# Optimization experiments

Measured on AMD Instinct MI355X. Metric: run time of the kernel, lower is better.

Reference implementation:

```python
import jax, jax.numpy as jnp
import numpy as np

LMAX, MMAX = 4, 2
C_IN, C_OUT = 128, 128           # sphere_channels, m_output_channels
NUM_EXPERTS = 8
NUM_SYSTEMS = 16
NUM_EDGES = 12288
M_SIZE = [LMAX + 1, 2 * (LMAX - 1 + 1), 2 * (LMAX - 2 + 1)]  # [5, 8, 6]


def _mole_linear(x, W, ce, b=None):
    """MoLE linear: per-edge expert mixing of weights, equivalently mixing of
    per-expert outputs.  x: [N, in] or [N, 2, in]; W: [K, in, out]; ce: [N, K]."""
    if x.ndim == 2:
        z = jnp.einsum('ni,kio->nko', x, W)        # [N, K, out]
        y = jnp.einsum('nk,nko->no', ce, z)
    else:
        z = jnp.einsum('nci,kio->nkco', x, W)      # [N, K, 2, out]
        y = jnp.einsum('nk,nkco->nco', ce, z)
    if b is not None:
        y = y + ce @ b                              # mixed bias, b: [K, out]
    return y


def setup_inputs() -> dict:
    key = jax.random.key(0)
    ks = jax.random.split(key, 8)
    num_mcoef = sum(M_SIZE)  # 19
    x = jax.random.normal(ks[0], (NUM_EDGES, num_mcoef, C_IN), dtype=jnp.float32)
    x_edge = jax.random.normal(ks[1], (NUM_EDGES, C_IN), dtype=jnp.float32)
    expert_coefficients = jax.random.uniform(ks[2], (NUM_SYSTEMS, NUM_EXPERTS), dtype=jnp.float32)
    edge_batch = jax.random.randint(ks[3], (NUM_EDGES,), 0, NUM_SYSTEMS)
    # fc_m0: in = (lmax+1)*C, out = (lmax+1)*C_out, with bias
    in0 = (LMAX + 1) * C_IN
    out0 = (LMAX + 1) * C_OUT
    W_m0 = jax.random.normal(ks[4], (NUM_EXPERTS, in0, out0), dtype=jnp.float32) * 0.02
    b_m0 = jnp.zeros((NUM_EXPERTS, out0), dtype=jnp.float32)
    # so2_m_conv m: in = (lmax-m+1)*C, out = 2*(lmax-m+1)*C_out, no bias
    nc1 = LMAX - 1 + 1
    W_m1 = jax.random.normal(ks[5], (NUM_EXPERTS, nc1 * C_IN, 2 * nc1 * C_OUT), dtype=jnp.float32) * 0.02
    nc2 = LMAX - 2 + 1
    W_m2 = jax.random.normal(ks[6], (NUM_EXPERTS, nc2 * C_IN, 2 * nc2 * C_OUT), dtype=jnp.float32) * 0.02
    return {
        'x': x, 'x_edge': x_edge,
        'expert_coefficients': expert_coefficients, 'edge_batch': edge_batch,
        'W_m0': W_m0, 'b_m0': b_m0, 'W_m1': W_m1, 'W_m2': W_m2,
    }


def reference(x, x_edge, expert_coefficients, edge_batch, W_m0, b_m0, W_m1, W_m2):
    N = x.shape[0]
    ce = expert_coefficients[edge_batch]               # [N, K] per-edge mix coeffs
    x0, x1, x2 = jnp.split(x, np.cumsum(M_SIZE[:-1]), axis=1)
    # m = 0 branch (internal_weights=True -> no radial rescale)
    y0 = _mole_linear(x0.reshape(N, -1), W_m0, ce, b_m0)
    out = [y0.reshape(N, -1, C_OUT)]                   # [N, lmax+1, C_out]
    # m >= 1 branches: SO(2) real/imag recombination
    for m, Wm, xm in ((1, W_m1, x1), (2, W_m2, x2)):
        nc = LMAX - m + 1
        xm = xm.reshape(N, 2, nc * C_IN)
        ym = _mole_linear(xm, Wm, ce)                  # [N, 2, 2*nc*C_out]
        ym = ym.reshape(N, 4, nc * C_OUT)
        x_m_r = ym[:, 0] - ym[:, 3]                    # x_r_0 - x_i_1
        x_m_i = ym[:, 2] + ym[:, 1]                    # x_r_1 + x_i_0
        out.append(x_m_r.reshape(N, nc, C_OUT))
        out.append(x_m_i.reshape(N, nc, C_OUT))
    return jnp.concatenate(out, axis=1)                # [N, 19, C_out]
```

## Files before the change

kernel.cpp:

```cpp
#include <hip/hip_runtime.h>
#include <cstdint>

#define N_EDGES 12288
#define ROWLEN  2432
#define CAP     2048

typedef __bf16 bf16;
typedef __bf16 bf16x8 __attribute__((ext_vector_type(8)));
typedef __bf16 bf16x4 __attribute__((ext_vector_type(4)));
typedef float  f32x4  __attribute__((ext_vector_type(4)));

#define ELEMS0 (640*640)
#define ELEMS1 (1024*1024)
#define ELEMS2 (768*768)

#define WS_IDX_OFF   1024
#define WS_BIAS_OFF  (WS_IDX_OFF + 16*CAP*4)
#define WS_W_OFF     (WS_BIAS_OFF + 16*640*4)
#define WZ_ELEMS     ((size_t)16*(ELEMS0+ELEMS1+ELEMS2))

template<int B> struct Cfg;
template<> struct Cfg<0> { static constexpr int K=640,  KS=640, XOFF=0,    NT=5;
                           static constexpr size_t WOFF=0; };
template<> struct Cfg<1> { static constexpr int K=1024, KS=512, XOFF=640,  NT=8;
                           static constexpr size_t WOFF=(size_t)16*ELEMS0; };
template<> struct Cfg<2> { static constexpr int K=768,  KS=384, XOFF=1664, NT=6;
                           static constexpr size_t WOFF=(size_t)16*ELEMS0+(size_t)16*ELEMS1; };

__device__ __forceinline__ void async_copy16(const void* g, void* l) {
  auto gp = reinterpret_cast<const __attribute__((address_space(1))) unsigned int*>(
      reinterpret_cast<uintptr_t>(g));
  auto lp = reinterpret_cast<__attribute__((address_space(3))) unsigned int*>(
      (unsigned int)reinterpret_cast<uintptr_t>(l));
  __builtin_amdgcn_global_load_lds(gp, lp, 16, 0, 0);
}

template<int B>
__device__ __forceinline__ void mix_body(const float* __restrict__ Wsrc,
                                         const float* ce_s,
                                         unsigned short* __restrict__ Wz, int pos) {
  constexpr int N = Cfg<B>::K, KS = Cfg<B>::KS, NT = N / 128, HALF = N / 2;
  constexpr int SRC_STRIDE = KS * N;
  constexpr size_t DST_STRIDE = (size_t)Cfg<B>::K * N;
  int nn = pos & 127, kgrp = (pos >> 7) & 3, rest = pos >> 9;
  int nt = rest % NT, kblk = rest / NT;
  int i0 = kblk * 32 + kgrp * 8;
  int c  = nt * 128 + nn;
  int si = i0, sc = c; float sg = 1.f;
  if (B > 0 && i0 >= KS) {
    si = i0 - KS;
    if (c < HALF) { sc = c + HALF; sg = -1.f; } else { sc = c - HALF; }
  }
  float w[8][8];
  const float* p0 = Wsrc + (size_t)si * N + sc;
#pragma unroll
  for (int e = 0; e < 8; ++e) {
    const float* p = p0 + (size_t)e * SRC_STRIDE;
#pragma unroll
    for (int j = 0; j < 8; ++j)
      w[e][j] = sg * p[(size_t)j * N];
  }
  unsigned short* db = Wz + Cfg<B>::WOFF + (size_t)pos * 8;
#pragma unroll
  for (int s = 0; s < 16; ++s) {
    float a[8] = {0, 0, 0, 0, 0, 0, 0, 0};
#pragma unroll
    for (int e = 0; e < 8; ++e) {
      float cc = ce_s[s * 8 + e];
#pragma unroll
      for (int j = 0; j < 8; ++j) a[j] += cc * w[e][j];
    }
    bf16x8 v;
#pragma unroll
    for (int j = 0; j < 8; ++j) v[j] = (bf16)a[j];
    *(bf16x8*)(db + s * DST_STRIDE) = v;
  }
}

__global__ __launch_bounds__(256) void prep_all(
    const float* __restrict__ W0, const float* __restrict__ W1,
    const float* __restrict__ W2, const float* __restrict__ ce,
    unsigned short* __restrict__ Wz,
    const int* __restrict__ eb, int* __restrict__ counts, int* __restrict__ idxb,
    const float* __restrict__ b0, float* __restrict__ bias) {
  __shared__ float ce_s[128];
  __shared__ int hcnt[16], hbase[16];
  int tid = threadIdx.x;
  int bx = blockIdx.x;
  if (bx < 1000) {
    if (tid < 128) ce_s[tid] = ce[tid];
    __syncthreads();
    if (bx < 200)      mix_body<0>(W0, ce_s, Wz, bx * 256 + tid);
    else if (bx < 712) mix_body<1>(W1, ce_s, Wz, (bx - 200) * 256 + tid);
    else               mix_body<2>(W2, ce_s, Wz, (bx - 712) * 256 + tid);
  } else if (bx < 1048) {
    int t = (bx - 1000) * 256 + tid;
    if (tid < 16) hcnt[tid] = 0;
    __syncthreads();
    int s = -1, lp = 0;
    if (t < N_EDGES) { s = eb[t]; lp = atomicAdd(&hcnt[s], 1); }
    __syncthreads();
    if (tid < 16) hbase[tid] = atomicAdd(counts + tid, hcnt[tid]);
    __syncthreads();
    if (s >= 0) { int p = hbase[s] + lp; if (p < CAP) idxb[s * CAP + p] = t; }
  } else {
    int t = (bx - 1048) * 256 + tid;
    int s = t / 640, c = t - s * 640;
    float a = 0.f;
#pragma unroll
    for (int e = 0; e < 8; ++e) a += ce[s * 8 + e] * b0[e * 640 + c];
    bias[t] = a;
  }
}

template<int B>
__device__ __forceinline__ void gemm_body(
    const float* __restrict__ x, const char* __restrict__ zeros,
    const unsigned short* __restrict__ Wz,
    const int* __restrict__ counts, const int* __restrict__ idxb,
    const float* __restrict__ bias, float* __restrict__ out,
    int s, int mt, int nt2, char* sm, int* eidx)
{
  constexpr int K = Cfg<B>::K, NT = Cfg<B>::NT, KB = K / 32, XOFF = Cfg<B>::XOFF;
  static_assert((K / 32) % 2 == 0, "KB must be even for the 2x-unrolled loop");
  int cnt = counts[s];
  int m0 = mt * 128;
  if (m0 >= cnt) return;
  int tid = threadIdx.x;
  if (tid < 128) eidx[tid] = (m0 + tid < cnt) ? idxb[s * CAP + m0 + tid] : -1;
  __syncthreads();
  char* Acur = sm;          char* Anxt = sm + 8192;
  char* Bc = sm + 16384;    char* Bm = sm + 32768;    char* Bn = sm + 49152;
  int wv = tid >> 6, ln = tid & 63;
  int wm = wv >> 1, wn = wv & 1;
  int kq = ln >> 4, lm = ln & 15;
  int c0 = nt2 * 2;
  int c16 = tid & 7, rbase = tid >> 3;
  int kq_w = c16 >> 1, half = c16 & 1;
  const char* arow4[4]; int kinc4[4];
#pragma unroll
  for (int i = 0; i < 4; ++i) {
    int e = eidx[rbase + 32 * i];
    if (e >= 0) { arow4[i] = (const char*)(x + (size_t)e * ROWLEN + XOFF); kinc4[i] = 128; }
    else        { arow4[i] = zeros; kinc4[i] = 0; }
  }
  const unsigned short* wb = Wz + Cfg<B>::WOFF + (size_t)s * K * K;

  auto loadA2 = [&](int kb, f32x4& r0, f32x4& r1, f32x4& r2, f32x4& r3)
      __attribute__((always_inline)) {
    r0 = *(const f32x4*)(arow4[0] + (size_t)kb * kinc4[0] + c16 * 16);
    r1 = *(const f32x4*)(arow4[1] + (size_t)kb * kinc4[1] + c16 * 16);
    r2 = *(const f32x4*)(arow4[2] + (size_t)kb * kinc4[2] + c16 * 16);
    r3 = *(const f32x4*)(arow4[3] + (size_t)kb * kinc4[3] + c16 * 16);
  };
  auto writeA2 = [&](char* dst, f32x4& r0, f32x4& r1, f32x4& r2, f32x4& r3)
      __attribute__((always_inline)) {
    f32x4 rr[4] = {r0, r1, r2, r3};
#pragma unroll
    for (int i = 0; i < 4; ++i) {
      int r = rbase + 32 * i;
      bf16x4 v;
      v[0] = (bf16)rr[i][0]; v[1] = (bf16)rr[i][1];
      v[2] = (bf16)rr[i][2]; v[3] = (bf16)rr[i][3];
      *(bf16x4*)(dst + kq_w * 2048 + ((r ^ (kq_w << 1)) * 16) + half * 8) = v;
    }
  };
  auto stageB = [&](int kb, char* dst) __attribute__((always_inline)) {
    const unsigned short* base = wb + (size_t)kb * (NT * 4096);
#pragma unroll
    for (int i = 0; i < 4; ++i) {
      int c = i * 256 + tid;
      int ck = c0 + (c >> 9); if (ck > NT - 1) ck = NT - 1;
      async_copy16(base + (size_t)ck * 4096 + (c & 511) * 8,
                   dst + (i * 256 + wv * 64) * 16);
    }
  };

  f32x4 acc[4][8];
#pragma unroll
  for (int i = 0; i < 4; ++i)
#pragma unroll
    for (int j = 0; j < 8; ++j) {
      acc[i][j][0] = 0.f; acc[i][j][1] = 0.f; acc[i][j][2] = 0.f; acc[i][j][3] = 0.f;
    }

  auto kstep = [&](int kb, f32x4& o0, f32x4& o1, f32x4& o2, f32x4& o3,
                           f32x4& n0, f32x4& n1, f32x4& n2, f32x4& n3)
      __attribute__((always_inline)) {
    if (kb + 2 < KB) {
      stageB(kb + 2, Bn);
      loadA2(kb + 2, n0, n1, n2, n3);
    }
    __builtin_amdgcn_sched_barrier(0);
    bf16x8 af[4], bq[8];
#pragma unroll
    for (int mi = 0; mi < 4; ++mi) {
      int r = wm * 64 + mi * 16 + lm;
      af[mi] = *(const bf16x8*)(Acur + kq * 2048 + ((r ^ (kq << 1)) * 16));
    }
#pragma unroll
    for (int ni = 0; ni < 8; ++ni)
      bq[ni] = *(const bf16x8*)(Bc + wn * 8192 + kq * 2048 + (ni * 16 + lm) * 16);
    __builtin_amdgcn_s_setprio(1);
#pragma unroll
    for (int mi = 0; mi < 4; ++mi)
#pragma unroll
      for (int ni = 0; ni < 8; ++ni)
        acc[mi][ni] = __builtin_amdgcn_mfma_f32_16x16x32_bf16(af[mi], bq[ni], acc[mi][ni], 0, 0, 0);
    __builtin_amdgcn_s_setprio(0);
    if (kb + 1 < KB)
      writeA2(Anxt, o0, o1, o2, o3);
    asm volatile("s_waitcnt lgkmcnt(0)" ::: "memory");
    __builtin_amdgcn_s_barrier();
    __builtin_amdgcn_sched_barrier(0);
    { char* t = Acur; Acur = Anxt; Anxt = t; }
    { char* tb = Bc; Bc = Bm; Bm = Bn; Bn = tb; }
  };

  f32x4 a0, a1, a2, a3, b0, b1, b2, b3;
  stageB(0, Bc);
  loadA2(0, a0, a1, a2, a3);
  writeA2(Acur, a0, a1, a2, a3);
  stageB(1, Bm);
  loadA2(1, a0, a1, a2, a3);
  asm volatile("s_waitcnt lgkmcnt(0)" ::: "memory");
  __builtin_amdgcn_s_barrier();
  __builtin_amdgcn_sched_barrier(0);

#pragma unroll 1
  for (int kb = 0; kb < KB; kb += 2) {
    kstep(kb,     a0, a1, a2, a3,  b0, b1, b2, b3);
    kstep(kb + 1, b0, b1, b2, b3,  a0, a1, a2, a3);
  }
  int cc = c0 + wn;
  if (cc >= NT) return;
  float bv[8] = {0, 0, 0, 0, 0, 0, 0, 0};
  if (B == 0) {
#pragma unroll
    for (int ni = 0; ni < 8; ++ni)
      bv[ni] = bias[s * 640 + cc * 128 + ni * 16 + lm];
  }
#pragma unroll
  for (int mi = 0; mi < 4; ++mi) {
#pragma unroll
    for (int r = 0; r < 4; ++r) {
      int row = wm * 64 + mi * 16 + kq * 4 + r;
      int e = eidx[row];
      if (e < 0) continue;
      float* po = out + (size_t)e * ROWLEN + XOFF + cc * 128 + lm;
#pragma unroll
      for (int ni = 0; ni < 8; ++ni) po[ni * 16] = acc[mi][ni][r] + bv[ni];
    }
  }
}

__global__ __launch_bounds__(256, 2) void gemm_all(
    const float* __restrict__ x, const char* __restrict__ zeros,
    const unsigned short* __restrict__ Wz,
    const int* __restrict__ counts, const int* __restrict__ idxb,
    const float* __restrict__ bias, float* __restrict__ out) {
  extern __shared__ char sm[];
  __shared__ int eidx[128];
  int g = blockIdx.x;
  int xcd = g & 7, j = g >> 3;
  int s = xcd + 8 * (j / 160);
  int r = j % 160;
  int mt = r / 10, bx = r % 10;
  if (bx < 3)      gemm_body<0>(x, zeros, Wz, counts, idxb, bias, out, s, mt, bx,     sm, eidx);
  else if (bx < 7) gemm_body<1>(x, zeros, Wz, counts, idxb, bias, out, s, mt, bx - 3, sm, eidx);
  else             gemm_body<2>(x, zeros, Wz, counts, idxb, bias, out, s, mt, bx - 7, sm, eidx);
}

extern "C" void kernel_launch(void* const* d_in, const int* in_sizes, int n_in,
                              void* d_out, int out_size, void* d_ws, size_t ws_size,
                              hipStream_t stream) {
  const float* x  = (const float*)d_in[0];
  const float* ce = (const float*)d_in[2];
  const int*   eb = (const int*)d_in[3];
  const float* W0 = (const float*)d_in[4];
  const float* b0 = (const float*)d_in[5];
  const float* W1 = (const float*)d_in[6];
  const float* W2 = (const float*)d_in[7];
  float* out = (float*)d_out;
  char* ws = (char*)d_ws;
  int*   counts = (int*)ws;
  char*  zeros  = ws + 256;
  int*   idxb   = (int*)(ws + WS_IDX_OFF);
  float* bias   = (float*)(ws + WS_BIAS_OFF);
  unsigned short* Wz = (unsigned short*)(ws + WS_W_OFF);

  hipMemsetAsync(ws, 0, 1024, stream);
  prep_all<<<1088, 256, 0, stream>>>(W0, W1, W2, ce, Wz, eb, counts, idxb, b0, bias);
  gemm_all<<<2560, 256, 65536, stream>>>(x, zeros, Wz, counts, idxb, bias, out);
}
```

Measured before the change: 352.9 us.

## Double waves per GEMM block, halving each wave's output tile

```diff
diff --git a/kernel.cpp b/kernel.cpp
--- a/kernel.cpp
+++ b/kernel.cpp
@@ -115,14 +115,13 @@
 
 template<int B>
 __device__ __forceinline__ void gemm_body(
-    const float* __restrict__ x, const char* __restrict__ zeros,
+    const float* __restrict__ x,
     const unsigned short* __restrict__ Wz,
     const int* __restrict__ counts, const int* __restrict__ idxb,
     const float* __restrict__ bias, float* __restrict__ out,
     int s, int mt, int nt2, char* sm, int* eidx)
 {
   constexpr int K = Cfg<B>::K, NT = Cfg<B>::NT, KB = K / 32, XOFF = Cfg<B>::XOFF;
-  static_assert((K / 32) % 2 == 0, "KB must be even for the 2x-unrolled loop");
   int cnt = counts[s];
   int m0 = mt * 128;
   if (m0 >= cnt) return;
@@ -132,113 +131,104 @@
   char* Acur = sm;          char* Anxt = sm + 8192;
   char* Bc = sm + 16384;    char* Bm = sm + 32768;    char* Bn = sm + 49152;
   int wv = tid >> 6, ln = tid & 63;
-  int wm = wv >> 1, wn = wv & 1;
+  int wm = wv >> 2, wn = wv & 3;
   int kq = ln >> 4, lm = ln & 15;
   int c0 = nt2 * 2;
   int c16 = tid & 7, rbase = tid >> 3;
   int kq_w = c16 >> 1, half = c16 & 1;
-  const char* arow4[4]; int kinc4[4];
-#pragma unroll
-  for (int i = 0; i < 4; ++i) {
-    int e = eidx[rbase + 32 * i];
-    if (e >= 0) { arow4[i] = (const char*)(x + (size_t)e * ROWLEN + XOFF); kinc4[i] = 128; }
-    else        { arow4[i] = zeros; kinc4[i] = 0; }
+  const char* xb = (const char*)x;
+  unsigned int aoff[2], kinc[2];
+#pragma unroll
+  for (int i = 0; i < 2; ++i) {
+    int e = eidx[rbase + 64 * i];
+    aoff[i] = (e >= 0) ? (unsigned int)(((size_t)e * ROWLEN + XOFF) * 4) : 0u;
+    kinc[i] = (e >= 0) ? 128u : 0u;
   }
   const unsigned short* wb = Wz + Cfg<B>::WOFF + (size_t)s * K * K;
 
-  auto loadA2 = [&](int kb, f32x4& r0, f32x4& r1, f32x4& r2, f32x4& r3)
-      __attribute__((always_inline)) {
-    r0 = *(const f32x4*)(arow4[0] + (size_t)kb * kinc4[0] + c16 * 16);
-    r1 = *(const f32x4*)(arow4[1] + (size_t)kb * kinc4[1] + c16 * 16);
-    r2 = *(const f32x4*)(arow4[2] + (size_t)kb * kinc4[2] + c16 * 16);
-    r3 = *(const f32x4*)(arow4[3] + (size_t)kb * kinc4[3] + c16 * 16);
+  f32x4 sreg[2];
+  auto loadA = [&](int kb) __attribute__((always_inline)) {
+#pragma unroll
+    for (int i = 0; i < 2; ++i)
+      sreg[i] = *(const f32x4*)(xb + aoff[i] + kb * kinc[i] + c16 * 16);
   };
-  auto writeA2 = [&](char* dst, f32x4& r0, f32x4& r1, f32x4& r2, f32x4& r3)
-      __attribute__((always_inline)) {
-    f32x4 rr[4] = {r0, r1, r2, r3};
-#pragma unroll
-    for (int i = 0; i < 4; ++i) {
-      int r = rbase + 32 * i;
+  auto writeA = [&](char* dst) __attribute__((always_inline)) {
+#pragma unroll
+    for (int i = 0; i < 2; ++i) {
+      int r = rbase + 64 * i;
       bf16x4 v;
-      v[0] = (bf16)rr[i][0]; v[1] = (bf16)rr[i][1];
-      v[2] = (bf16)rr[i][2]; v[3] = (bf16)rr[i][3];
+      v[0] = (bf16)sreg[i][0]; v[1] = (bf16)sreg[i][1];
+      v[2] = (bf16)sreg[i][2]; v[3] = (bf16)sreg[i][3];
       *(bf16x4*)(dst + kq_w * 2048 + ((r ^ (kq_w << 1)) * 16) + half * 8) = v;
     }
   };
   auto stageB = [&](int kb, char* dst) __attribute__((always_inline)) {
     const unsigned short* base = wb + (size_t)kb * (NT * 4096);
 #pragma unroll
-    for (int i = 0; i < 4; ++i) {
-      int c = i * 256 + tid;
+    for (int i = 0; i < 2; ++i) {
+      int c = i * 512 + tid;
       int ck = c0 + (c >> 9); if (ck > NT - 1) ck = NT - 1;
       async_copy16(base + (size_t)ck * 4096 + (c & 511) * 8,
-                   dst + (i * 256 + wv * 64) * 16);
+                   dst + (i * 512 + wv * 64) * 16);
     }
   };
 
-  f32x4 acc[4][8];
+  f32x4 acc[4][4];
 #pragma unroll
   for (int i = 0; i < 4; ++i)
 #pragma unroll
-    for (int j = 0; j < 8; ++j) {
+    for (int j = 0; j < 4; ++j) {
       acc[i][j][0] = 0.f; acc[i][j][1] = 0.f; acc[i][j][2] = 0.f; acc[i][j][3] = 0.f;
     }
 
-  auto kstep = [&](int kb, f32x4& o0, f32x4& o1, f32x4& o2, f32x4& o3,
-                           f32x4& n0, f32x4& n1, f32x4& n2, f32x4& n3)
-      __attribute__((always_inline)) {
-    if (kb + 2 < KB) {
-      stageB(kb + 2, Bn);
-      loadA2(kb + 2, n0, n1, n2, n3);
-    }
+  stageB(0, Bc);
+  loadA(0);
+  writeA(Acur);
+  stageB(1, Bm);
+  loadA(1);
+  asm volatile("s_waitcnt lgkmcnt(0)" ::: "memory");
+  __builtin_amdgcn_s_barrier();
+  __builtin_amdgcn_sched_barrier(0);
+
+#pragma unroll 1
+  for (int kb = 0; kb < KB; ++kb) {
+    if (kb + 2 < KB) stageB(kb + 2, Bn);
     __builtin_amdgcn_sched_barrier(0);
-    bf16x8 af[4], bq[8];
+    bf16x8 af[4], bq[4];
 #pragma unroll
     for (int mi = 0; mi < 4; ++mi) {
       int r = wm * 64 + mi * 16 + lm;
       af[mi] = *(const bf16x8*)(Acur + kq * 2048 + ((r ^ (kq << 1)) * 16));
     }
 #pragma unroll
-    for (int ni = 0; ni < 8; ++ni)
-      bq[ni] = *(const bf16x8*)(Bc + wn * 8192 + kq * 2048 + (ni * 16 + lm) * 16);
+    for (int ni = 0; ni < 4; ++ni)
+      bq[ni] = *(const bf16x8*)(Bc + (wn >> 1) * 8192 + kq * 2048 +
+                                (((wn & 1) * 64 + ni * 16 + lm) * 16));
     __builtin_amdgcn_s_setprio(1);
 #pragma unroll
     for (int mi = 0; mi < 4; ++mi)
 #pragma unroll
-      for (int ni = 0; ni < 8; ++ni)
+      for (int ni = 0; ni < 4; ++ni)
         acc[mi][ni] = __builtin_amdgcn_mfma_f32_16x16x32_bf16(af[mi], bq[ni], acc[mi][ni], 0, 0, 0);
     __builtin_amdgcn_s_setprio(0);
-    if (kb + 1 < KB)
-      writeA2(Anxt, o0, o1, o2, o3);
+    if (kb + 1 < KB) {
+      writeA(Anxt);
+      if (kb + 2 < KB) loadA(kb + 2);
+    }
     asm volatile("s_waitcnt lgkmcnt(0)" ::: "memory");
     __builtin_amdgcn_s_barrier();
     __builtin_amdgcn_sched_barrier(0);
     { char* t = Acur; Acur = Anxt; Anxt = t; }
     { char* tb = Bc; Bc = Bm; Bm = Bn; Bn = tb; }
-  };
-
-  f32x4 a0, a1, a2, a3, b0, b1, b2, b3;
-  stageB(0, Bc);
-  loadA2(0, a0, a1, a2, a3);
-  writeA2(Acur, a0, a1, a2, a3);
-  stageB(1, Bm);
-  loadA2(1, a0, a1, a2, a3);
-  asm volatile("s_waitcnt lgkmcnt(0)" ::: "memory");
-  __builtin_amdgcn_s_barrier();
-  __builtin_amdgcn_sched_barrier(0);
-
-#pragma unroll 1
-  for (int kb = 0; kb < KB; kb += 2) {
-    kstep(kb,     a0, a1, a2, a3,  b0, b1, b2, b3);
-    kstep(kb + 1, b0, b1, b2, b3,  a0, a1, a2, a3);
-  }
-  int cc = c0 + wn;
+  }
+  int cc = c0 + (wn >> 1);
   if (cc >= NT) return;
-  float bv[8] = {0, 0, 0, 0, 0, 0, 0, 0};
+  int colb = cc * 128 + (wn & 1) * 64;
+  float bv[4] = {0, 0, 0, 0};
   if (B == 0) {
 #pragma unroll
-    for (int ni = 0; ni < 8; ++ni)
-      bv[ni] = bias[s * 640 + cc * 128 + ni * 16 + lm];
+    for (int ni = 0; ni < 4; ++ni)
+      bv[ni] = bias[s * 640 + colb + ni * 16 + lm];
   }
 #pragma unroll
   for (int mi = 0; mi < 4; ++mi) {
@@ -247,15 +237,15 @@
       int row = wm * 64 + mi * 16 + kq * 4 + r;
       int e = eidx[row];
       if (e < 0) continue;
-      float* po = out + (size_t)e * ROWLEN + XOFF + cc * 128 + lm;
-#pragma unroll
-      for (int ni = 0; ni < 8; ++ni) po[ni * 16] = acc[mi][ni][r] + bv[ni];
-    }
-  }
-}
-
-__global__ __launch_bounds__(256, 2) void gemm_all(
-    const float* __restrict__ x, const char* __restrict__ zeros,
+      float* po = out + (size_t)e * ROWLEN + XOFF + colb + lm;
+#pragma unroll
+      for (int ni = 0; ni < 4; ++ni) po[ni * 16] = acc[mi][ni][r] + bv[ni];
+    }
+  }
+}
+
+__global__ __launch_bounds__(512, 4) void gemm_all(
+    const float* __restrict__ x,
     const unsigned short* __restrict__ Wz,
     const int* __restrict__ counts, const int* __restrict__ idxb,
     const float* __restrict__ bias, float* __restrict__ out) {
@@ -266,9 +256,9 @@
   int s = xcd + 8 * (j / 160);
   int r = j % 160;
   int mt = r / 10, bx = r % 10;
-  if (bx < 3)      gemm_body<0>(x, zeros, Wz, counts, idxb, bias, out, s, mt, bx,     sm, eidx);
-  else if (bx < 7) gemm_body<1>(x, zeros, Wz, counts, idxb, bias, out, s, mt, bx - 3, sm, eidx);
-  else             gemm_body<2>(x, zeros, Wz, counts, idxb, bias, out, s, mt, bx - 7, sm, eidx);
+  if (bx < 3)      gemm_body<0>(x, Wz, counts, idxb, bias, out, s, mt, bx,     sm, eidx);
+  else if (bx < 7) gemm_body<1>(x, Wz, counts, idxb, bias, out, s, mt, bx - 3, sm, eidx);
+  else             gemm_body<2>(x, Wz, counts, idxb, bias, out, s, mt, bx - 7, sm, eidx);
 }
 
 extern "C" void kernel_launch(void* const* d_in, const int* in_sizes, int n_in,
@@ -284,12 +274,11 @@
   float* out = (float*)d_out;
   char* ws = (char*)d_ws;
   int*   counts = (int*)ws;
-  char*  zeros  = ws + 256;
   int*   idxb   = (int*)(ws + WS_IDX_OFF);
   float* bias   = (float*)(ws + WS_BIAS_OFF);
   unsigned short* Wz = (unsigned short*)(ws + WS_W_OFF);
 
   hipMemsetAsync(ws, 0, 1024, stream);
   prep_all<<<1088, 256, 0, stream>>>(W0, W1, W2, ce, Wz, eb, counts, idxb, b0, bias);
-  gemm_all<<<2560, 256, 65536, stream>>>(x, zeros, Wz, counts, idxb, bias, out);
-}
+  gemm_all<<<2560, 512, 65536, stream>>>(x, Wz, counts, idxb, bias, out);
+}
```

Measured after the change: 320.2 us. 9.3% less time.
